# Kernel tuning notes

Measured on AMD Instinct MI355X. Metric: run time of the kernel, lower is better.

Reference implementation:

```python
import jax, jax.numpy as jnp
import numpy as np

B, P, NOBJ, C = 32, 16384, 50, 21
THRESHOLD, NEG_POS_RATIO, ALPHA = 0.5, 3.0, 1.0


def cxcy_to_xy(c):
    return jnp.concatenate([c[:, :2] - c[:, 2:] / 2, c[:, :2] + c[:, 2:] / 2], axis=1)


def xy_to_cxcy(xy):
    return jnp.concatenate([(xy[:, :2] + xy[:, 2:]) / 2, xy[:, 2:] - xy[:, :2]], axis=1)


def cxcy_to_gcxgcy(cxcy, priors_cxcy):
    # standard SSD encoding with variances 0.1 / 0.2
    g_cxcy = (cxcy[:, :2] - priors_cxcy[:, :2]) / (priors_cxcy[:, 2:] / 10.0)
    g_wh = jnp.log(cxcy[:, 2:] / priors_cxcy[:, 2:]) * 5.0
    return jnp.concatenate([g_cxcy, g_wh], axis=1)


def jaccard(a, b):
    # a: [N,4] xyxy, b: [P,4] xyxy -> [N,P]
    lt = jnp.maximum(a[:, None, :2], b[None, :, :2])
    rb = jnp.minimum(a[:, None, 2:], b[None, :, 2:])
    inter = jnp.clip(rb - lt, 0.0).prod(-1)
    area_a = (a[:, 2:] - a[:, :2]).prod(-1)
    area_b = (b[:, 2:] - b[:, :2]).prod(-1)
    return inter / (area_a[:, None] + area_b[None, :] - inter)


def setup_inputs() -> dict:
    key = jax.random.key(0)
    k1, k2, k3, k4, k5, k6, k7 = jax.random.split(key, 7)
    predicted_locs = jax.random.normal(k1, (B, P, 4), dtype=jnp.float32)
    predicted_scores = jax.random.normal(k2, (B, P, C), dtype=jnp.float32)
    # ground-truth boxes: valid xyxy in [0,1] with positive extent
    ccx = jax.random.uniform(k3, (B, NOBJ, 2), minval=0.1, maxval=0.9)
    wh = jax.random.uniform(k4, (B, NOBJ, 2), minval=0.02, maxval=0.2)
    boxes = jnp.concatenate([ccx - wh / 2, ccx + wh / 2], axis=-1).astype(jnp.float32)
    labels = jax.random.randint(k5, (B, NOBJ), 1, C)  # object labels are >= 1 (0 = background)
    pcxy = jax.random.uniform(k6, (P, 2), minval=0.05, maxval=0.95)
    pwh = jax.random.uniform(k7, (P, 2), minval=0.02, maxval=0.4)
    priors_cxcy = jnp.concatenate([pcxy, pwh], axis=-1).astype(jnp.float32)
    return dict(predicted_locs=predicted_locs, predicted_scores=predicted_scores,
                boxes=boxes, labels=labels, priors_cxcy=priors_cxcy)


def reference(predicted_locs, predicted_scores, boxes, labels, priors_cxcy):
    priors_xy = cxcy_to_xy(priors_cxcy)

    def assign(boxes_i, labels_i):
        ov = jaccard(boxes_i, priors_xy)                    # [N,P]
        overlap_for_prior = ov.max(axis=0)                  # [P]
        object_for_prior = ov.argmax(axis=0)                # [P]
        prior_for_object = ov.argmax(axis=1)                # [N]
        # force each object to own its best prior
        object_for_prior = object_for_prior.at[prior_for_object].set(jnp.arange(NOBJ))
        overlap_for_prior = overlap_for_prior.at[prior_for_object].set(1.0)
        label_for_prior = labels_i[object_for_prior]
        label_for_prior = jnp.where(overlap_for_prior < THRESHOLD, 0, label_for_prior)
        assigned_xy = boxes_i[object_for_prior]             # [P,4]
        true_locs_i = cxcy_to_gcxgcy(xy_to_cxcy(assigned_xy), priors_cxcy)
        return true_locs_i, label_for_prior

    true_locs, true_classes = jax.vmap(assign)(boxes, labels)  # [B,P,4], [B,P]

    pos = true_classes != 0                                 # [B,P]
    n_pos = pos.sum(axis=1)                                 # [B]
    n_pos_total = n_pos.sum().astype(jnp.float32)

    # nn.L1Loss(): mean abs error over positive prior entries (Npos*4 elements)
    l1 = jnp.abs(predicted_locs - true_locs) * pos[..., None]
    loc_loss = l1.sum() / (n_pos_total * 4.0)

    # per-prior cross entropy
    logp = jax.nn.log_softmax(predicted_scores, axis=-1)    # [B,P,C]
    ce = -jnp.take_along_axis(logp, true_classes[..., None], axis=-1)[..., 0]  # [B,P]

    conf_pos = jnp.where(pos, ce, 0.0).sum()
    neg = jnp.where(pos, 0.0, ce)
    neg_sorted = -jnp.sort(-neg, axis=1)                    # descending per image
    ranks = jnp.arange(P)[None, :].astype(jnp.float32)
    hard = ranks < (NEG_POS_RATIO * n_pos.astype(jnp.float32))[:, None]
    conf_hard_neg = jnp.where(hard, neg_sorted, 0.0).sum()

    conf_loss = (conf_hard_neg + conf_pos) / n_pos_total
    return conf_loss + ALPHA * loc_loss
```

## Files before the change

### kernel.cpp

```cpp
#include <hip/hip_runtime.h>
#include <hip/hip_bf16.h>
#include <float.h>

#define BB   32
#define PP   16384
#define NOBJ 50
#define NCLS 21
#define PBLK 64
#define NBLK (BB * PBLK)


__global__ __launch_bounds__(256) void k_iou(
    const float* __restrict__ boxes, const float* __restrict__ priors,
    unsigned long long* __restrict__ bp_part,
    unsigned long long* __restrict__ ovk)
{
#pragma clang fp contract(off)
    const int b     = (int)blockIdx.x / 28;
    const int r     = (int)blockIdx.x % 28;
    const int n0    = (r >> 2) * 8;
    const int chunk = r & 3;
    const int pbase = chunk << 12;
    const int t     = (int)threadIdx.x;
    const float4* gpri = reinterpret_cast<const float4*>(priors);

    __shared__ unsigned long long sbest[8];
    if (t < 8) sbest[t] = 0ull;

    float ax0[8], ay0[8], ax1[8], ay1[8], aarea[8];
    unsigned lo[8];
#pragma unroll
    for (int k = 0; k < 8; ++k) {
        int nn = n0 + k; if (nn >= NOBJ) nn = NOBJ - 1;
        float4 bx = reinterpret_cast<const float4*>(boxes)[b * NOBJ + nn];
        ax0[k] = bx.x; ay0[k] = bx.y; ax1[k] = bx.z; ay1[k] = bx.w;
        aarea[k] = (bx.z - bx.x) * (bx.w - bx.y);
        lo[k] = (unsigned)(NOBJ - 1 - nn);
    }

    unsigned long long bk[8];
#pragma unroll
    for (int k = 0; k < 8; ++k) bk[k] = 0ull;

#pragma unroll 2
    for (int j = 0; j < 16; ++j) {
        int p = pbase + t + (j << 8);
        float4 pc = gpri[p];
        float hx = pc.z / 2.0f, hy = pc.w / 2.0f;
        float px0 = pc.x - hx, py0 = pc.y - hy;
        float px1 = pc.x + hx, py1 = pc.y + hy;
        float areab = (px1 - px0) * (py1 - py0);
        unsigned inv = 0xFFFFFFFFu - (unsigned)p;
        unsigned long long pb = 0ull;
#pragma unroll
        for (int k = 0; k < 8; ++k) {
            float ltx = fmaxf(ax0[k], px0), lty = fmaxf(ay0[k], py0);
            float rbx = fminf(ax1[k], px1), rby = fminf(ay1[k], py1);
            float dx = fmaxf(rbx - ltx, 0.0f);
            float dy = fmaxf(rby - lty, 0.0f);
            float inter = dx * dy;
            float iou = __fdividef(inter, (aarea[k] + areab) - inter);
            unsigned long long hib = (unsigned long long)__float_as_uint(iou) << 32;
            unsigned long long keyo = hib | (unsigned long long)inv;
            if (keyo > bk[k]) bk[k] = keyo;
            unsigned long long keyp = hib | (unsigned long long)lo[k];
            if (keyp > pb) pb = keyp;
        }
        atomicMax(&ovk[b * PP + p], pb);
    }
    __syncthreads();
#pragma unroll
    for (int k = 0; k < 8; ++k) {
        unsigned long long v = bk[k];
        for (int o = 32; o > 0; o >>= 1) {
            unsigned long long other = __shfl_down(v, o, 64);
            if (other > v) v = other;
        }
        if ((t & 63) == 0) atomicMax(&sbest[k], v);
    }
    __syncthreads();
    if (t < 8 && n0 + t < NOBJ)
        bp_part[chunk * BB * NOBJ + b * NOBJ + n0 + t] = sbest[t];
}

__global__ __launch_bounds__(256) void k_main(
    const float* __restrict__ locs, const float* __restrict__ scores,
    const float* __restrict__ boxes, const int* __restrict__ labels,
    const float* __restrict__ priors,
    const unsigned long long* __restrict__ bp_part,
    const unsigned long long* __restrict__ ovk,
    float* __restrict__ neg, double* __restrict__ pc_conf,
    double* __restrict__ pc_loc, int* __restrict__ pc_npos)
{
#pragma clang fp contract(off)
    const int b   = (int)blockIdx.x >> 6;
    const int p0  = ((int)blockIdx.x & 63) << 8;
    const int t   = (int)threadIdx.x;
    const int p   = p0 + t;
    const int idx = b * PP + p;

    __shared__ float  sls[256 * NCLS];
    __shared__ int    sforce[256];
    __shared__ float4 sbox[NOBJ];
    __shared__ int    slab[NOBJ];
    __shared__ double sconf[4], sloc[4];
    __shared__ int    snp[4];

    {
        const float4* gsc = reinterpret_cast<const float4*>(
            scores + (size_t)(b * PP + p0) * NCLS);
        float4* dls = reinterpret_cast<float4*>(sls);
#pragma unroll
        for (int i = 0; i < 6; ++i) {
            int j = i * 256 + t;
            if (j < (256 * NCLS) / 4) dls[j] = gsc[j];
        }
    }
    sforce[t] = -1;
    if (t < NOBJ) {
        sbox[t] = reinterpret_cast<const float4*>(boxes)[b * NOBJ + t];
        slab[t] = labels[b * NOBJ + t];
    }
    __syncthreads();
    if (t < NOBJ) {
        unsigned long long k0 = bp_part[0 * BB * NOBJ + b * NOBJ + t];
        unsigned long long k1 = bp_part[1 * BB * NOBJ + b * NOBJ + t];
        unsigned long long k2 = bp_part[2 * BB * NOBJ + b * NOBJ + t];
        unsigned long long k3 = bp_part[3 * BB * NOBJ + b * NOBJ + t];
        if (k1 > k0) k0 = k1;
        if (k3 > k2) k2 = k3;
        if (k2 > k0) k0 = k2;
        int spf = (int)(0xFFFFFFFFu - (unsigned)(k0 & 0xFFFFFFFFull));
        if (spf >= p0 && spf < p0 + 256)
            atomicMax(&sforce[spf - p0], t);
    }
    __syncthreads();

    unsigned long long key = ovk[idx];
    int   bestn = NOBJ - 1 - (int)((unsigned)key & 63u);
    float v     = __uint_as_float((unsigned)(key >> 32));
    int fn = sforce[t];
    if (fn >= 0) { bestn = fn; v = 1.0f; }

    int lbl = slab[bestn];
    if (v < 0.5f) lbl = 0;
    const bool pos = (lbl != 0);

    float locl1 = 0.0f;
    if (pos) {
        float4 bx = sbox[bestn];
        float4 pc = reinterpret_cast<const float4*>(priors)[p];
        float cx = (bx.x + bx.z) / 2.0f;
        float cy = (bx.y + bx.w) / 2.0f;
        float w  = bx.z - bx.x, h = bx.w - bx.y;
        float gx = (cx - pc.x) / (pc.z / 10.0f);
        float gy = (cy - pc.y) / (pc.w / 10.0f);
        float gw = logf(w / pc.z) * 5.0f;
        float gh = logf(h / pc.w) * 5.0f;
        float4 pl = reinterpret_cast<const float4*>(locs)[idx];
        locl1 = fabsf(pl.x - gx) + fabsf(pl.y - gy) +
                fabsf(pl.z - gw) + fabsf(pl.w - gh);
    }

    float x[NCLS];
    float m = -FLT_MAX;
#pragma unroll
    for (int c = 0; c < NCLS; ++c) { x[c] = sls[t * NCLS + c]; m = fmaxf(m, x[c]); }
    float tgt = sls[t * NCLS + lbl];
    float s = 0.0f;
#pragma unroll
    for (int c = 0; c < NCLS; ++c) s += expf(x[c] - m);
    float ce = (logf(s) + m) - tgt;

    neg[idx] = pos ? 0.0f : ce;

    float cp = pos ? ce : 0.0f;
    unsigned long long bal = __ballot(pos);
    float s1 = cp, s2 = locl1;
    for (int o = 32; o > 0; o >>= 1) {
        s1 += __shfl_down(s1, o, 64);
        s2 += __shfl_down(s2, o, 64);
    }
    if ((t & 63) == 0) {
        int w = t >> 6;
        sconf[w] = (double)s1;
        sloc[w]  = (double)s2;
        snp[w]   = (int)__popcll(bal);
    }
    __syncthreads();
    if (t == 0) {
        pc_conf[blockIdx.x] = sconf[0] + sconf[1] + sconf[2] + sconf[3];
        pc_loc[blockIdx.x]  = sloc[0] + sloc[1] + sloc[2] + sloc[3];
        pc_npos[blockIdx.x] = snp[0] + snp[1] + snp[2] + snp[3];
    }
}

__global__ __launch_bounds__(1024) void k_topk(
    const float* __restrict__ neg, const int* __restrict__ pc_npos,
    double* __restrict__ hard)
{
    const int b    = (int)blockIdx.x;
    const int t    = (int)threadIdx.x;
    const int lane = t & 63;
    const int wid  = t >> 6;

    __shared__ unsigned hist[64 * 257];
    __shared__ unsigned ssuf[256];
    __shared__ unsigned s_bb, s_above;
    __shared__ float swave[16];
    __shared__ int s_np;

    if (t < 64) {
        int v = pc_npos[b * PBLK + t];
        for (int o = 32; o > 0; o >>= 1) v += __shfl_down(v, o, 64);
        if (t == 0) s_np = v;
    }

    float v[16];
    {
        const float4* g = reinterpret_cast<const float4*>(neg + (size_t)b * PP);
#pragma unroll
        for (int i = 0; i < 4; ++i) {
            float4 q = g[i * 1024 + t];
            v[i*4+0] = q.x; v[i*4+1] = q.y; v[i*4+2] = q.z; v[i*4+3] = q.w;
        }
    }
    __syncthreads();

    long long K = 3LL * (long long)s_np;
    if (K > PP) K = PP;
    unsigned remaining = (unsigned)K;
    unsigned prefix = 0, mask = 0;
    float mySum = 0.0f;

    for (int shift = 24; shift >= 0; shift -= 8) {
        for (int i = t; i < 64 * 257; i += 1024) hist[i] = 0;
        __syncthreads();
        unsigned* h = hist + lane * 257;
#pragma unroll
        for (int i = 0; i < 16; ++i) {
            unsigned u = __float_as_uint(v[i]);
            if ((u & mask) == prefix) atomicAdd(&h[(u >> shift) & 255u], 1u);
        }
        __syncthreads();
        unsigned cnt = 0;
        if (t < 256) {
#pragma unroll
            for (int w = 0; w < 64; ++w) cnt += hist[w * 257 + t];
            ssuf[t] = cnt;
        }
        __syncthreads();
        for (int off = 1; off < 256; off <<= 1) {
            unsigned add = 0;
            if (t < 256 && t + off < 256) add = ssuf[t + off];
            __syncthreads();
            if (t < 256) ssuf[t] += add;
            __syncthreads();
        }
        if (t < 256) {
            unsigned suf = ssuf[t];
            if (suf >= remaining && suf - cnt < remaining) {
                s_bb = (unsigned)t; s_above = suf - cnt;
            }
        }
        __syncthreads();
        unsigned bb = s_bb;
#pragma unroll
        for (int i = 0; i < 16; ++i) {
            unsigned u = __float_as_uint(v[i]);
            if ((u & mask) == prefix && ((u >> shift) & 255u) > bb)
                mySum += v[i];
        }
        remaining -= s_above;
        prefix |= bb << shift;
        mask   |= 255u << shift;
        __syncthreads();
    }

    float s = mySum;
    for (int o = 32; o > 0; o >>= 1) s += __shfl_down(s, o, 64);
    if ((t & 63) == 0) swave[wid] = s;
    __syncthreads();
    if (t == 0) {
        float tot = 0.0f;
        for (int w = 0; w < 16; ++w) tot += swave[w];
        if (remaining) tot += (float)remaining * __uint_as_float(prefix);
        hard[b] = (double)tot;
    }
}

__global__ __launch_bounds__(256) void k_final(
    const double* __restrict__ pc_conf, const double* __restrict__ pc_loc,
    const int* __restrict__ pc_npos, const double* __restrict__ hard,
    float* __restrict__ out)
{
    const int t = (int)threadIdx.x;
    __shared__ double sa[4], sb[4], sh[4];
    __shared__ int sn[4];
    double a = 0.0, c = 0.0, h = 0.0; int np = 0;
    for (int i = t; i < NBLK; i += 256) {
        a += pc_conf[i]; c += pc_loc[i]; np += pc_npos[i];
    }
    if (t < BB) h = hard[t];
    for (int o = 32; o > 0; o >>= 1) {
        a += __shfl_down(a, o, 64);
        c += __shfl_down(c, o, 64);
        h += __shfl_down(h, o, 64);
        np += __shfl_down(np, o, 64);
    }
    if ((t & 63) == 0) { int w = t >> 6; sa[w]=a; sb[w]=c; sh[w]=h; sn[w]=np; }
    __syncthreads();
    if (t == 0) {
        double at = sa[0]+sa[1]+sa[2]+sa[3];
        double ct = sb[0]+sb[1]+sb[2]+sb[3];
        double ht = sh[0]+sh[1]+sh[2]+sh[3];
        double npt = (double)(sn[0]+sn[1]+sn[2]+sn[3]);
        out[0] = (float)((at + ht) / npt + ct / (npt * 4.0));
    }
}

extern "C" void kernel_launch(void* const* d_in, const int* in_sizes, int n_in,
                              void* d_out, int out_size, void* d_ws, size_t ws_size,
                              hipStream_t stream) {
    const float* locs   = (const float*)d_in[0];
    const float* scores = (const float*)d_in[1];
    const float* boxes  = (const float*)d_in[2];
    const int*   labels = (const int*)d_in[3];
    const float* priors = (const float*)d_in[4];

    char* ws = (char*)d_ws;
    unsigned long long* bp_part = (unsigned long long*)ws;
    double* pc_conf = (double*)(ws + 65536);
    double* pc_loc  = (double*)(ws + 81920);
    int*    pc_npos = (int*)(ws + 98304);
    double* hard    = (double*)(ws + 106496);
    unsigned long long* ovk = (unsigned long long*)(ws + 131072);
    float*  neg     = (float*)(ws + 4456448);
    float*  out     = (float*)d_out;

    hipMemsetAsync(ovk, 0, (size_t)BB * PP * 8, stream);
    hipLaunchKernelGGL(k_iou,   dim3(BB * 28), dim3(256),  0, stream,
                       boxes, priors, bp_part, ovk);
    hipLaunchKernelGGL(k_main,  dim3(NBLK),    dim3(256),  0, stream,
                       locs, scores, boxes, labels, priors, bp_part, ovk,
                       neg, pc_conf, pc_loc, pc_npos);
    hipLaunchKernelGGL(k_topk,  dim3(BB),      dim3(1024), 0, stream,
                       neg, pc_npos, hard);
    hipLaunchKernelGGL(k_final, dim3(1),       dim3(256),  0, stream,
                       pc_conf, pc_loc, pc_npos, hard, out);
}
```

Baseline: 83.29 us.

## Replace per-prior atomicMax with per-group partial buffers and finer IoU chunking

The IoU kernel no longer issues 64-bit atomicMax into a zeroed global array, so the memset is dropped. Each object group now writes its own per-prior best key into a partial buffer, and k_main reduces the seven partials. The grid is also split into 16 prior chunks of 1024 with 4 priors per thread, which gives more blocks. The trade-off is more global traffic (7 partial arrays written and read, about 29MB) and a 16-way reduction of the per-object best, in exchange for removing atomics and the memset launch.

```diff
diff --git a/kernel.cpp b/kernel.cpp
--- a/kernel.cpp
+++ b/kernel.cpp
@@ -8,70 +8,85 @@
 #define NCLS 21
 #define PBLK 64
 #define NBLK (BB * PBLK)
+#define NGRP 7
+#define NCHK 16
+#define CPRI 1024
+#define JPT  4
 
 
 __global__ __launch_bounds__(256) void k_iou(
     const float* __restrict__ boxes, const float* __restrict__ priors,
     unsigned long long* __restrict__ bp_part,
-    unsigned long long* __restrict__ ovk)
+    unsigned long long* __restrict__ ovp_part)
 {
 #pragma clang fp contract(off)
-    const int b     = (int)blockIdx.x / 28;
-    const int r     = (int)blockIdx.x % 28;
-    const int n0    = (r >> 2) * 8;
-    const int chunk = r & 3;
-    const int pbase = chunk << 12;
+    const int blk   = (int)blockIdx.x;
+    const int b     = blk / (NGRP * NCHK);
+    const int rem   = blk % (NGRP * NCHK);
+    const int g     = rem / NCHK;
+    const int c     = rem % NCHK;
+    const int n0    = g * 8;
+    const int pbase = c * CPRI;
     const int t     = (int)threadIdx.x;
-    const float4* gpri = reinterpret_cast<const float4*>(priors);
 
     __shared__ unsigned long long sbest[8];
     if (t < 8) sbest[t] = 0ull;
 
     float ax0[8], ay0[8], ax1[8], ay1[8], aarea[8];
-    unsigned lo[8];
 #pragma unroll
     for (int k = 0; k < 8; ++k) {
         int nn = n0 + k; if (nn >= NOBJ) nn = NOBJ - 1;
         float4 bx = reinterpret_cast<const float4*>(boxes)[b * NOBJ + nn];
         ax0[k] = bx.x; ay0[k] = bx.y; ax1[k] = bx.z; ay1[k] = bx.w;
         aarea[k] = (bx.z - bx.x) * (bx.w - bx.y);
-        lo[k] = (unsigned)(NOBJ - 1 - nn);
-    }
-
-    unsigned long long bk[8];
-#pragma unroll
-    for (int k = 0; k < 8; ++k) bk[k] = 0ull;
-
-#pragma unroll 2
-    for (int j = 0; j < 16; ++j) {
-        int p = pbase + t + (j << 8);
-        float4 pc = gpri[p];
+    }
+
+    float px0[JPT], py0[JPT], px1[JPT], py1[JPT], pab[JPT];
+#pragma unroll
+    for (int j = 0; j < JPT; ++j) {
+        float4 pc = reinterpret_cast<const float4*>(priors)[pbase + t + j * 256];
         float hx = pc.z / 2.0f, hy = pc.w / 2.0f;
-        float px0 = pc.x - hx, py0 = pc.y - hy;
-        float px1 = pc.x + hx, py1 = pc.y + hy;
-        float areab = (px1 - px0) * (py1 - py0);
-        unsigned inv = 0xFFFFFFFFu - (unsigned)p;
-        unsigned long long pb = 0ull;
-#pragma unroll
-        for (int k = 0; k < 8; ++k) {
-            float ltx = fmaxf(ax0[k], px0), lty = fmaxf(ay0[k], py0);
-            float rbx = fminf(ax1[k], px1), rby = fminf(ay1[k], py1);
+        px0[j] = pc.x - hx; py0[j] = pc.y - hy;
+        px1[j] = pc.x + hx; py1[j] = pc.y + hy;
+        pab[j] = (px1[j] - px0[j]) * (py1[j] - py0[j]);
+    }
+
+    float bof[8];  int bop[8];
+    float bpf[JPT]; int bpn[JPT];
+#pragma unroll
+    for (int k = 0; k < 8; ++k) { bof[k] = -1.0f; bop[k] = 0; }
+#pragma unroll
+    for (int j = 0; j < JPT; ++j) { bpf[j] = -1.0f; bpn[j] = 0; }
+
+#pragma unroll
+    for (int k = 0; k < 8; ++k) {
+#pragma unroll
+        for (int j = 0; j < JPT; ++j) {
+            float ltx = fmaxf(ax0[k], px0[j]), lty = fmaxf(ay0[k], py0[j]);
+            float rbx = fminf(ax1[k], px1[j]), rby = fminf(ay1[k], py1[j]);
             float dx = fmaxf(rbx - ltx, 0.0f);
             float dy = fmaxf(rby - lty, 0.0f);
             float inter = dx * dy;
-            float iou = __fdividef(inter, (aarea[k] + areab) - inter);
-            unsigned long long hib = (unsigned long long)__float_as_uint(iou) << 32;
-            unsigned long long keyo = hib | (unsigned long long)inv;
-            if (keyo > bk[k]) bk[k] = keyo;
-            unsigned long long keyp = hib | (unsigned long long)lo[k];
-            if (keyp > pb) pb = keyp;
-        }
-        atomicMax(&ovk[b * PP + p], pb);
-    }
+            float iou = __fdividef(inter, (aarea[k] + pab[j]) - inter);
+            if (iou > bof[k]) { bof[k] = iou; bop[k] = pbase + t + j * 256; }
+            if (iou > bpf[j]) { bpf[j] = iou; bpn[j] = n0 + k; }
+        }
+    }
+
+#pragma unroll
+    for (int j = 0; j < JPT; ++j) {
+        unsigned long long key =
+            ((unsigned long long)__float_as_uint(bpf[j]) << 32) |
+            (unsigned long long)(unsigned)(NOBJ - 1 - bpn[j]);
+        ovp_part[((size_t)g * BB + b) * PP + pbase + t + j * 256] = key;
+    }
+
     __syncthreads();
 #pragma unroll
     for (int k = 0; k < 8; ++k) {
-        unsigned long long v = bk[k];
+        unsigned long long v =
+            ((unsigned long long)__float_as_uint(bof[k]) << 32) |
+            (unsigned long long)(0xFFFFFFFFu - (unsigned)bop[k]);
         for (int o = 32; o > 0; o >>= 1) {
             unsigned long long other = __shfl_down(v, o, 64);
             if (other > v) v = other;
@@ -80,7 +95,7 @@
     }
     __syncthreads();
     if (t < 8 && n0 + t < NOBJ)
-        bp_part[chunk * BB * NOBJ + b * NOBJ + n0 + t] = sbest[t];
+        bp_part[(size_t)c * BB * NOBJ + b * NOBJ + n0 + t] = sbest[t];
 }
 
 __global__ __launch_bounds__(256) void k_main(
@@ -88,7 +103,7 @@
     const float* __restrict__ boxes, const int* __restrict__ labels,
     const float* __restrict__ priors,
     const unsigned long long* __restrict__ bp_part,
-    const unsigned long long* __restrict__ ovk,
+    const unsigned long long* __restrict__ ovp_part,
     float* __restrict__ neg, double* __restrict__ pc_conf,
     double* __restrict__ pc_loc, int* __restrict__ pc_npos)
 {
@@ -123,20 +138,24 @@
     }
     __syncthreads();
     if (t < NOBJ) {
-        unsigned long long k0 = bp_part[0 * BB * NOBJ + b * NOBJ + t];
-        unsigned long long k1 = bp_part[1 * BB * NOBJ + b * NOBJ + t];
-        unsigned long long k2 = bp_part[2 * BB * NOBJ + b * NOBJ + t];
-        unsigned long long k3 = bp_part[3 * BB * NOBJ + b * NOBJ + t];
-        if (k1 > k0) k0 = k1;
-        if (k3 > k2) k2 = k3;
-        if (k2 > k0) k0 = k2;
+        unsigned long long k0 = bp_part[b * NOBJ + t];
+#pragma unroll
+        for (int cc = 1; cc < NCHK; ++cc) {
+            unsigned long long kc = bp_part[(size_t)cc * BB * NOBJ + b * NOBJ + t];
+            if (kc > k0) k0 = kc;
+        }
         int spf = (int)(0xFFFFFFFFu - (unsigned)(k0 & 0xFFFFFFFFull));
         if (spf >= p0 && spf < p0 + 256)
             atomicMax(&sforce[spf - p0], t);
     }
     __syncthreads();
 
-    unsigned long long key = ovk[idx];
+    unsigned long long key = ovp_part[(size_t)b * PP + p];
+#pragma unroll
+    for (int g = 1; g < NGRP; ++g) {
+        unsigned long long kg = ovp_part[((size_t)g * BB + b) * PP + p];
+        if (kg > key) key = kg;
+    }
     int   bestn = NOBJ - 1 - (int)((unsigned)key & 63u);
     float v     = __uint_as_float((unsigned)(key >> 32));
     int fn = sforce[t];
@@ -330,22 +349,21 @@
 
     char* ws = (char*)d_ws;
     unsigned long long* bp_part = (unsigned long long*)ws;
-    double* pc_conf = (double*)(ws + 65536);
-    double* pc_loc  = (double*)(ws + 81920);
-    int*    pc_npos = (int*)(ws + 98304);
-    double* hard    = (double*)(ws + 106496);
-    unsigned long long* ovk = (unsigned long long*)(ws + 131072);
-    float*  neg     = (float*)(ws + 4456448);
+    double* pc_conf = (double*)(ws + 262144);
+    double* pc_loc  = (double*)(ws + 278528);
+    int*    pc_npos = (int*)(ws + 294912);
+    double* hard    = (double*)(ws + 303104);
+    unsigned long long* ovp_part = (unsigned long long*)(ws + 327680);
+    float*  neg     = (float*)(ws + 33554432);
     float*  out     = (float*)d_out;
 
-    hipMemsetAsync(ovk, 0, (size_t)BB * PP * 8, stream);
-    hipLaunchKernelGGL(k_iou,   dim3(BB * 28), dim3(256),  0, stream,
-                       boxes, priors, bp_part, ovk);
-    hipLaunchKernelGGL(k_main,  dim3(NBLK),    dim3(256),  0, stream,
-                       locs, scores, boxes, labels, priors, bp_part, ovk,
+    hipLaunchKernelGGL(k_iou,   dim3(BB * NGRP * NCHK), dim3(256),  0, stream,
+                       boxes, priors, bp_part, ovp_part);
+    hipLaunchKernelGGL(k_main,  dim3(NBLK),             dim3(256),  0, stream,
+                       locs, scores, boxes, labels, priors, bp_part, ovp_part,
                        neg, pc_conf, pc_loc, pc_npos);
-    hipLaunchKernelGGL(k_topk,  dim3(BB),      dim3(1024), 0, stream,
+    hipLaunchKernelGGL(k_topk,  dim3(BB),               dim3(1024), 0, stream,
                        neg, pc_npos, hard);
-    hipLaunchKernelGGL(k_final, dim3(1),       dim3(256),  0, stream,
+    hipLaunchKernelGGL(k_final, dim3(1),                dim3(256),  0, stream,
                        pc_conf, pc_loc, pc_npos, hard, out);
 }
```

After: 80.95 us. 1.03x faster.
